# Kernel tuning notes

Measured on AMD Instinct MI355X. Metric: run time of the kernel, lower is better.

## Reference

```python
import jax, jax.numpy as jnp
import numpy as np

SIGMAS = (1.0, 2.0, 3.0, 4.0, 5.0)
ALPHAS = jnp.asarray([0.1, 0.2, 0.3, 0.4, 0.5], dtype=jnp.float32)
KSIZE = 7
PAD = KSIZE // 2  # 3, reflect padding


def _gaussian_kernels():
    # matches torch: x = arange(-ks//2+1, ks//2+1) = [-3..3]
    x = np.arange(-KSIZE // 2 + 1, KSIZE // 2 + 1, dtype=np.float32)
    ks = []
    for s in SIGMAS:
        g = np.exp(-x ** 2 / (2.0 * s ** 2))
        k = np.outer(g, g)
        k /= k.sum()
        ks.append(k)
    # depthwise conv kernels: (H, 1, 7, 7), OIHW with feature_group_count=H
    return jnp.asarray(np.stack(ks)[:, None, :, :])


def setup_inputs() -> dict:
    key = jax.random.key(0)
    ks = jax.random.split(key, 5)
    B, N, C = 8, 1024, 320
    return {
        "x": jax.random.normal(ks[0], (B, N, C), dtype=jnp.float32),
        "ln_g": jnp.ones((C,), dtype=jnp.float32),
        "ln_b": jnp.zeros((C,), dtype=jnp.float32),
        "qkv_w": jax.random.normal(ks[1], (3 * C, C), dtype=jnp.float32) * 0.02,
        "qkv_b": jax.random.normal(ks[2], (3 * C,), dtype=jnp.float32) * 0.02,
        "proj_w": jax.random.normal(ks[3], (C, C), dtype=jnp.float32) * 0.02,
        "proj_b": jax.random.normal(ks[4], (C,), dtype=jnp.float32) * 0.02,
    }


def reference(x, ln_g, ln_b, qkv_w, qkv_b, proj_w, proj_b):
    B, N, C = x.shape
    H = 5
    d = C // H
    kernels = _gaussian_kernels()  # (H,1,7,7), fixed buffers

    # LayerNorm
    mu = jnp.mean(x, axis=-1, keepdims=True)
    var = jnp.var(x, axis=-1, keepdims=True)
    xn = (x - mu) * jax.lax.rsqrt(var + 1e-5) * ln_g + ln_b

    # QKV projection -> (3, B, H, N, d)
    qkv = (xn @ qkv_w.T + qkv_b).reshape(B, N, 3, H, d).transpose(2, 0, 3, 1, 4)
    q, k, v = qkv[0], qkv[1], qkv[2]

    # attention scores (B, H, N, N)
    attn = jnp.einsum("bhnd,bhmd->bhnm", q, k) * (d ** -0.5)

    # per-head Gaussian blur as depthwise conv with reflect padding
    padded = jnp.pad(attn, ((0, 0), (0, 0), (PAD, PAD), (PAD, PAD)), mode="reflect")
    blurred = jax.lax.conv_general_dilated(
        padded, kernels, window_strides=(1, 1), padding="VALID",
        dimension_numbers=("NCHW", "OIHW", "NCHW"), feature_group_count=H)

    combined = jax.nn.softmax(attn + ALPHAS[None, :, None, None] * blurred, axis=-1)

    out = jnp.einsum("bhnm,bhmd->bhnd", combined, v)  # (B,H,N,d)
    out = out.transpose(0, 2, 1, 3).reshape(B, N, C)
    return out @ proj_w.T + proj_b
```

## Files before the change

### kernel.cpp

```cpp
#include <hip/hip_runtime.h>
#include <math.h>

#define B_ 8
#define N_ 1024
#define C_ 320
#define H_ 5
#define D_ 64
#define M_ (B_*N_)

typedef unsigned short ushort_t;
typedef _Float16 half_t;
typedef __attribute__((ext_vector_type(2))) _Float16 h2;
typedef __attribute__((ext_vector_type(8))) _Float16 f16x8;
typedef __attribute__((ext_vector_type(4))) float f32x4;

__device__ __forceinline__ ushort_t f2h(float f) {
  union { half_t h; ushort_t u; } c; c.h = (half_t)f; return c.u;
}
__device__ __forceinline__ unsigned pkrtz(float a, float b) {
  auto r = __builtin_amdgcn_cvt_pkrtz(a, b);
  union { decltype(r) v; unsigned u; } c; c.v = r; return c.u;
}

__global__ __launch_bounds__(256) void prep_kernel(
    const float* __restrict__ qkv_w, const float* __restrict__ proj_w,
    const float* __restrict__ x, const float* __restrict__ gamma,
    const float* __restrict__ beta,
    ushort_t* __restrict__ wqb, ushort_t* __restrict__ wpb,
    ushort_t* __restrict__ xnb) {
  int bid = blockIdx.x;
  int tid = threadIdx.x;
  if (bid < 200) {
    const float* src = bid < 150 ? qkv_w : proj_w;
    ushort_t* dst    = bid < 150 ? wqb   : wpb;
    int base = (bid < 150 ? bid : bid - 150) * 2048;
    int idx = base + tid*8;
    float4 x0 = *(const float4*)(src+idx);
    float4 x1 = *(const float4*)(src+idx+4);
    unsigned pk[4] = {pkrtz(x0.x,x0.y), pkrtz(x0.z,x0.w),
                      pkrtz(x1.x,x1.y), pkrtz(x1.z,x1.w)};
    *(uint4*)(dst+idx) = *(const uint4*)pk;
  } else {
    int row = (bid - 200)*4 + (tid >> 6);
    int lane = tid & 63;
    const float* xr = x + (long)row * C_;
    float vals[5];
    float s = 0.f, ss = 0.f;
#pragma unroll
    for (int j = 0; j < 5; ++j) {
      float vv = xr[lane + 64*j];
      vals[j] = vv; s += vv; ss += vv*vv;
    }
#pragma unroll
    for (int o = 32; o > 0; o >>= 1) {
      s  += __shfl_xor(s, o, 64);
      ss += __shfl_xor(ss, o, 64);
    }
    float mean = s * (1.0f/C_);
    float var  = ss * (1.0f/C_) - mean*mean;
    float rstd = rsqrtf(var + 1e-5f);
    ushort_t* outr = xnb + (long)row * C_;
#pragma unroll
    for (int j = 0; j < 5; ++j) {
      int c = lane + 64*j;
      outr[c] = f2h((vals[j]-mean)*rstd*gamma[c] + beta[c]);
    }
  }
}

__global__ __launch_bounds__(256) void qkvm_kernel(const ushort_t* __restrict__ xnb,
    const ushort_t* __restrict__ wqb, const float* __restrict__ bias,
    ushort_t* __restrict__ q, ushort_t* __restrict__ k, ushort_t* __restrict__ vt) {
  __shared__ __align__(16) ushort_t As[128][72];
  __shared__ __align__(16) ushort_t Bs[64][72];
  __shared__ __align__(16) ushort_t Vs[64][136];
  int j0 = blockIdx.x * 64;
  int m0 = blockIdx.y * 128;
  int tid = threadIdx.x;
  int lane = tid & 63, wv = tid >> 6;
  int l16 = lane & 15, qd = lane >> 4;
  f32x4 acc[2][4];
#pragma unroll
  for (int i=0;i<2;++i)
#pragma unroll
    for (int j=0;j<4;++j) acc[i][j] = (f32x4){0.f,0.f,0.f,0.f};
  for (int kk = 0; kk < C_; kk += 64) {
#pragma unroll
    for (int i = 0; i < 4; ++i) {
      int idx = tid + 256*i;
      int row = idx >> 3, c8 = (idx & 7) << 3;
      *(uint4*)&As[row][c8] = *(const uint4*)(xnb + (long)(m0+row)*C_ + kk + c8);
    }
    {
      int idx = tid;
      int row = idx >> 3, c8 = (idx & 7) << 3;
      *(uint4*)&Bs[row][c8] = *(const uint4*)(wqb + (long)(j0+row)*C_ + kk + c8);
      idx = tid + 256; row = idx >> 3; c8 = (idx & 7) << 3;
      *(uint4*)&Bs[row][c8] = *(const uint4*)(wqb + (long)(j0+row)*C_ + kk + c8);
    }
    __syncthreads();
#pragma unroll
    for (int kb = 0; kb < 2; ++kb) {
      int ko = kb*32 + qd*8;
      f16x8 a0 = *(const f16x8*)&As[wv*32 + l16][ko];
      f16x8 a1 = *(const f16x8*)&As[wv*32 + 16 + l16][ko];
#pragma unroll
      for (int ct = 0; ct < 4; ++ct) {
        f16x8 b = *(const f16x8*)&Bs[ct*16 + l16][ko];
        acc[0][ct] = __builtin_amdgcn_mfma_f32_16x16x32_f16(a0, b, acc[0][ct], 0,0,0);
        acc[1][ct] = __builtin_amdgcn_mfma_f32_16x16x32_f16(a1, b, acc[1][ct], 0,0,0);
      }
    }
    __syncthreads();
  }
  int three = j0 / 320;
  int rembase = j0 - three*320;
  if (three < 2) {
    ushort_t* dst = three == 0 ? q : k;
    float scale = three == 0 ? 0.125f : 1.0f;
#pragma unroll
    for (int rt = 0; rt < 2; ++rt)
#pragma unroll
      for (int ct = 0; ct < 4; ++ct) {
        int rem = rembase + ct*16 + l16;
        int h = rem >> 6, dd = rem & 63;
        float bi = bias[j0 + ct*16 + l16];
#pragma unroll
        for (int r = 0; r < 4; ++r) {
          int m = m0 + wv*32 + rt*16 + qd*4 + r;
          int b = m >> 10, n = m & (N_-1);
          dst[(((long)b*H_ + h)*N_ + n)*D_ + dd] = f2h((acc[rt][ct][r] + bi) * scale);
        }
      }
  } else {
    int h = rembase >> 6;
#pragma unroll
    for (int rt = 0; rt < 2; ++rt)
#pragma unroll
      for (int ct = 0; ct < 4; ++ct) {
        float bi = bias[j0 + ct*16 + l16];
#pragma unroll
        for (int r = 0; r < 4; ++r) {
          int col = wv*32 + rt*16 + qd*4 + r;
          Vs[ct*16 + l16][col] = f2h(acc[rt][ct][r] + bi);
        }
      }
    __syncthreads();
    int b = m0 >> 10, n0b = m0 & (N_-1);
#pragma unroll
    for (int i = 0; i < 4; ++i) {
      int idx = tid + 256*i;
      int row = idx >> 4, c8 = (idx & 15) << 3;
      *(uint4*)(vt + (((long)b*H_ + h)*D_ + row)*N_ + n0b + c8) = *(const uint4*)&Vs[row][c8];
    }
  }
}

__global__ __launch_bounds__(512) void qb_kernel(
    const ushort_t* __restrict__ q, const ushort_t* __restrict__ kk,
    ushort_t* __restrict__ qb, ushort_t* __restrict__ kb) {
  int bh = blockIdx.y;
  int h = bh % H_;
  int r = blockIdx.x*64 + (threadIdx.x >> 3);
  int d8 = (threadIdx.x & 7) << 3;
  float sigma = (float)(h + 1);
  float ei = -1.f / (2.f * sigma * sigma);
  float ga = expf(9.f*ei), gb = expf(4.f*ei), gc = expf(1.f*ei);
  float isum = 1.f / (2.f*(ga + gb + gc) + 1.f);
  float alpha = 0.1f * sigma;
  const float w[7] = {ga*isum, gb*isum, gc*isum, isum, gc*isum, gb*isum, ga*isum};
  const ushort_t* qb_base = q  + (long)bh*N_*D_ + d8;
  const ushort_t* kb_base = kk + (long)bh*N_*D_ + d8;
  float aq[8] = {0,0,0,0,0,0,0,0};
  float ak[8] = {0,0,0,0,0,0,0,0};
#pragma unroll
  for (int t = 0; t < 7; ++t) {
    int p = r + t - 3;
    int rr = p < 0 ? -p : (p > N_-1 ? 2*(N_-1)-p : p);
    union { uint4 v; h2 hh[4]; } uq, uk;
    uq.v = *(const uint4*)(qb_base + (long)rr*D_);
    uk.v = *(const uint4*)(kb_base + (long)rr*D_);
    float wt = w[t];
#pragma unroll
    for (int j = 0; j < 4; ++j) {
      aq[2*j]   += wt * (float)uq.hh[j].x;
      aq[2*j+1] += wt * (float)uq.hh[j].y;
      ak[2*j]   += wt * (float)uk.hh[j].x;
      ak[2*j+1] += wt * (float)uk.hh[j].y;
    }
  }
  ushort_t pq[8], pk[8];
#pragma unroll
  for (int j = 0; j < 8; ++j) {
    pq[j] = f2h(aq[j]);
    pk[j] = f2h(ak[j] * alpha);
  }
  long ooff = ((long)bh*N_ + r)*D_ + d8;
  *(uint4*)(qb + ooff) = *(const uint4*)pq;
  *(uint4*)(kb + ooff) = *(const uint4*)pk;
}

__global__ __launch_bounds__(256, 2) void bsp_kernel(
    const ushort_t* __restrict__ q,  const ushort_t* __restrict__ qbb,
    const ushort_t* __restrict__ kk, const ushort_t* __restrict__ kb,
    const ushort_t* __restrict__ vt, ushort_t* __restrict__ aob) {
  __shared__ __align__(16) ushort_t Ks[2][64][72];
  __shared__ __align__(16) ushort_t Bs[2][64][72];
  __shared__ __align__(16) ushort_t Vs[2][64][72];
  __shared__ __align__(16) ushort_t Pb[4][16][72];

  int lin = blockIdx.x;
  int lin2 = (lin & 7)*80 + (lin >> 3);
  int bh = lin2 >> 4;
  int qblk = lin2 & 15;
  int h = bh % H_;
  int bb = bh / H_;
  int tid = threadIdx.x;
  int wv = tid >> 6, lane = tid & 63;
  int l16 = lane & 15, qd = lane >> 4;
  int qbase = qblk*64 + wv*16;

  int srow = tid >> 3, sc8 = (tid & 7) << 3;
  const ushort_t* kgp = kk + (long)bh*N_*D_ + (long)srow*D_ + sc8;
  const ushort_t* bgp = kb + (long)bh*N_*D_ + (long)srow*D_ + sc8;
  const ushort_t* vgp = vt + (long)bh*D_*N_ + (long)srow*N_ + sc8;

  long qoff = ((long)bh*N_ + qbase + l16)*D_ + qd*8;
  f16x8 bq0 = *(const f16x8*)(q   + qoff);
  f16x8 bq1 = *(const f16x8*)(q   + qoff + 32);
  f16x8 bq2 = *(const f16x8*)(qbb + qoff);
  f16x8 bq3 = *(const f16x8*)(qbb + qoff + 32);

  ushort_t (*Pw)[72] = Pb[wv];
  float rsum = 0.f;
  f32x4 oa[4];
#pragma unroll
  for (int dt = 0; dt < 4; ++dt) oa[dt] = (f32x4){0.f,0.f,0.f,0.f};

  {
    uint4 k0 = *(const uint4*)(kgp);
    uint4 k1 = *(const uint4*)(kgp + 32*D_);
    uint4 b0 = *(const uint4*)(bgp);
    uint4 b1 = *(const uint4*)(bgp + 32*D_);
    uint4 v0 = *(const uint4*)(vgp);
    uint4 v1 = *(const uint4*)(vgp + 32*N_);
    *(uint4*)&Ks[0][srow][sc8]    = k0;
    *(uint4*)&Ks[0][srow+32][sc8] = k1;
    *(uint4*)&Bs[0][srow][sc8]    = b0;
    *(uint4*)&Bs[0][srow+32][sc8] = b1;
    *(uint4*)&Vs[0][srow][sc8]    = v0;
    *(uint4*)&Vs[0][srow+32][sc8] = v1;
  }
  __syncthreads();

  for (int ch = 0; ch < 16; ++ch) {
    const int cur = ch & 1, nxt = cur ^ 1;
    uint4 gk0, gk1, gb0, gb1, gv0, gv1;
    if (ch < 15) {
      int c1 = (ch + 1) * 64;
      gk0 = *(const uint4*)(kgp + (long)c1*D_);
      gk1 = *(const uint4*)(kgp + (long)(c1+32)*D_);
      gb0 = *(const uint4*)(bgp + (long)c1*D_);
      gb1 = *(const uint4*)(bgp + (long)(c1+32)*D_);
      gv0 = *(const uint4*)(vgp + c1);
      gv1 = *(const uint4*)(vgp + 32*N_ + c1);
    }
#pragma unroll
    for (int kt = 0; kt < 4; ++kt) {
      int r = kt*16 + l16;
      f16x8 a0 = *(const f16x8*)&Ks[cur][r][qd*8];
      f16x8 a1 = *(const f16x8*)&Ks[cur][r][qd*8 + 32];
      f16x8 a2 = *(const f16x8*)&Bs[cur][r][qd*8];
      f16x8 a3 = *(const f16x8*)&Bs[cur][r][qd*8 + 32];
      f32x4 s = (f32x4){0.f,0.f,0.f,0.f};
      s = __builtin_amdgcn_mfma_f32_16x16x32_f16(a0, bq0, s, 0,0,0);
      s = __builtin_amdgcn_mfma_f32_16x16x32_f16(a1, bq1, s, 0,0,0);
      s = __builtin_amdgcn_mfma_f32_16x16x32_f16(a2, bq2, s, 0,0,0);
      s = __builtin_amdgcn_mfma_f32_16x16x32_f16(a3, bq3, s, 0,0,0);
      float e0 = __expf(s[0]), e1 = __expf(s[1]);
      float e2 = __expf(s[2]), e3 = __expf(s[3]);
      rsum += (e0 + e1) + (e2 + e3);
      *(uint2*)&Pw[l16][kt*16 + qd*4] = make_uint2(pkrtz(e0,e1), pkrtz(e2,e3));
    }
#pragma unroll
    for (int ks = 0; ks < 2; ++ks) {
      f16x8 af = *(const f16x8*)&Pw[l16][ks*32 + qd*8];
#pragma unroll
      for (int dt = 0; dt < 4; ++dt) {
        f16x8 bf = *(const f16x8*)&Vs[cur][dt*16 + l16][ks*32 + qd*8];
        oa[dt] = __builtin_amdgcn_mfma_f32_16x16x32_f16(af, bf, oa[dt], 0,0,0);
      }
    }
    if (ch < 15) {
      *(uint4*)&Ks[nxt][srow][sc8]    = gk0;
      *(uint4*)&Ks[nxt][srow+32][sc8] = gk1;
      *(uint4*)&Bs[nxt][srow][sc8]    = gb0;
      *(uint4*)&Bs[nxt][srow+32][sc8] = gb1;
      *(uint4*)&Vs[nxt][srow][sc8]    = gv0;
      *(uint4*)&Vs[nxt][srow+32][sc8] = gv1;
    }
    __syncthreads();
  }

  rsum += __shfl_xor(rsum, 16, 64);
  rsum += __shfl_xor(rsum, 32, 64);
  float rinv = 1.f / rsum;
  float rv[4];
#pragma unroll
  for (int r = 0; r < 4; ++r) rv[r] = __shfl(rinv, qd*4 + r, 64);
#pragma unroll
  for (int dt = 0; dt < 4; ++dt)
#pragma unroll
    for (int r = 0; r < 4; ++r)
      aob[((long)(bb*N_ + qbase + qd*4 + r))*C_ + h*64 + dt*16 + l16] =
          f2h(oa[dt][r] * rv[r]);
}

__global__ __launch_bounds__(256) void projm_kernel(const ushort_t* __restrict__ aob,
    const ushort_t* __restrict__ wpb, const float* __restrict__ bias,
    float* __restrict__ out) {
  __shared__ __align__(16) ushort_t As[128][72];
  __shared__ __align__(16) ushort_t Bs[64][72];
  int j0 = blockIdx.x * 64;
  int m0 = blockIdx.y * 128;
  int tid = threadIdx.x;
  int lane = tid & 63, wv = tid >> 6;
  int l16 = lane & 15, qd = lane >> 4;
  f32x4 acc[2][4];
#pragma unroll
  for (int i=0;i<2;++i)
#pragma unroll
    for (int j=0;j<4;++j) acc[i][j] = (f32x4){0.f,0.f,0.f,0.f};
  for (int kk = 0; kk < C_; kk += 64) {
#pragma unroll
    for (int i = 0; i < 4; ++i) {
      int idx = tid + 256*i;
      int row = idx >> 3, c8 = (idx & 7) << 3;
      *(uint4*)&As[row][c8] = *(const uint4*)(aob + (long)(m0+row)*C_ + kk + c8);
    }
    {
      int idx = tid;
      int row = idx >> 3, c8 = (idx & 7) << 3;
      *(uint4*)&Bs[row][c8] = *(const uint4*)(wpb + (long)(j0+row)*C_ + kk + c8);
      idx = tid + 256; row = idx >> 3; c8 = (idx & 7) << 3;
      *(uint4*)&Bs[row][c8] = *(const uint4*)(wpb + (long)(j0+row)*C_ + kk + c8);
    }
    __syncthreads();
#pragma unroll
    for (int kb = 0; kb < 2; ++kb) {
      int ko = kb*32 + qd*8;
      f16x8 a0 = *(const f16x8*)&As[wv*32 + l16][ko];
      f16x8 a1 = *(const f16x8*)&As[wv*32 + 16 + l16][ko];
#pragma unroll
      for (int ct = 0; ct < 4; ++ct) {
        f16x8 b = *(const f16x8*)&Bs[ct*16 + l16][ko];
        acc[0][ct] = __builtin_amdgcn_mfma_f32_16x16x32_f16(a0, b, acc[0][ct], 0,0,0);
        acc[1][ct] = __builtin_amdgcn_mfma_f32_16x16x32_f16(a1, b, acc[1][ct], 0,0,0);
      }
    }
    __syncthreads();
  }
#pragma unroll
  for (int rt = 0; rt < 2; ++rt)
#pragma unroll
    for (int ct = 0; ct < 4; ++ct) {
      float bi = bias[j0 + ct*16 + l16];
#pragma unroll
      for (int r = 0; r < 4; ++r) {
        int m = m0 + wv*32 + rt*16 + qd*4 + r;
        out[(long)m*C_ + j0 + ct*16 + l16] = acc[rt][ct][r] + bi;
      }
    }
}

extern "C" void kernel_launch(void* const* d_in, const int* in_sizes, int n_in,
                              void* d_out, int out_size, void* d_ws, size_t ws_size,
                              hipStream_t stream) {
  const float* x      = (const float*)d_in[0];
  const float* ln_g   = (const float*)d_in[1];
  const float* ln_b   = (const float*)d_in[2];
  const float* qkv_w  = (const float*)d_in[3];
  const float* qkv_b  = (const float*)d_in[4];
  const float* proj_w = (const float*)d_in[5];
  const float* proj_b = (const float*)d_in[6];
  float* out = (float*)d_out;

  char* ws = (char*)d_ws;
  const long sz_bhnd = (long)B_*H_*N_*D_;
  ushort_t* xnb  = (ushort_t*)ws;                   ws += (long)M_*C_*2;
  ushort_t* aob  = (ushort_t*)ws;                   ws += (long)M_*C_*2;
  ushort_t* q    = (ushort_t*)ws;                   ws += sz_bhnd*2;
  ushort_t* k    = (ushort_t*)ws;                   ws += sz_bhnd*2;
  ushort_t* vt   = (ushort_t*)ws;                   ws += sz_bhnd*2;
  ushort_t* qb   = (ushort_t*)ws;                   ws += sz_bhnd*2;
  ushort_t* kb   = (ushort_t*)ws;                   ws += sz_bhnd*2;
  ushort_t* wqb  = (ushort_t*)ws;                   ws += (long)3*C_*C_*2;
  ushort_t* wpb  = (ushort_t*)ws;                   ws += (long)C_*C_*2;

  prep_kernel<<<2248, 256, 0, stream>>>(qkv_w, proj_w, x, ln_g, ln_b, wqb, wpb, xnb);
  qkvm_kernel<<<dim3(15, 64), 256, 0, stream>>>(xnb, wqb, qkv_b, q, k, vt);
  qb_kernel<<<dim3(16, B_*H_), 512, 0, stream>>>(q, k, qb, kb);
  bsp_kernel<<<640, 256, 0, stream>>>(q, qb, k, kb, vt, aob);
  projm_kernel<<<dim3(5, 64), 256, 0, stream>>>(aob, wpb, proj_b, out);
}
```

Measured before the change: 139.2 us.

## Register-prefetch GEMM tiles and single-buffer attention LDS for higher occupancy

Result: slower. 188.7 us (+35.6%).

```diff
diff --git a/kernel.cpp b/kernel.cpp
--- a/kernel.cpp
+++ b/kernel.cpp
@@ -84,19 +84,46 @@
   for (int i=0;i<2;++i)
 #pragma unroll
     for (int j=0;j<4;++j) acc[i][j] = (f32x4){0.f,0.f,0.f,0.f};
-  for (int kk = 0; kk < C_; kk += 64) {
+
+  uint4 rA[4], rB[2];
+#pragma unroll
+  for (int i = 0; i < 4; ++i) {
+    int idx = tid + 256*i;
+    int row = idx >> 3, c8 = (idx & 7) << 3;
+    rA[i] = *(const uint4*)(xnb + (long)(m0+row)*C_ + c8);
+  }
+  {
+    int idx = tid, row = idx >> 3, c8 = (idx & 7) << 3;
+    rB[0] = *(const uint4*)(wqb + (long)(j0+row)*C_ + c8);
+    idx = tid + 256; row = idx >> 3; c8 = (idx & 7) << 3;
+    rB[1] = *(const uint4*)(wqb + (long)(j0+row)*C_ + c8);
+  }
+  for (int kt5 = 0; kt5 < 5; ++kt5) {
+    __syncthreads();
 #pragma unroll
     for (int i = 0; i < 4; ++i) {
       int idx = tid + 256*i;
       int row = idx >> 3, c8 = (idx & 7) << 3;
-      *(uint4*)&As[row][c8] = *(const uint4*)(xnb + (long)(m0+row)*C_ + kk + c8);
+      *(uint4*)&As[row][c8] = rA[i];
     }
     {
-      int idx = tid;
-      int row = idx >> 3, c8 = (idx & 7) << 3;
-      *(uint4*)&Bs[row][c8] = *(const uint4*)(wqb + (long)(j0+row)*C_ + kk + c8);
+      int idx = tid, row = idx >> 3, c8 = (idx & 7) << 3;
+      *(uint4*)&Bs[row][c8] = rB[0];
       idx = tid + 256; row = idx >> 3; c8 = (idx & 7) << 3;
-      *(uint4*)&Bs[row][c8] = *(const uint4*)(wqb + (long)(j0+row)*C_ + kk + c8);
+      *(uint4*)&Bs[row][c8] = rB[1];
+    }
+    if (kt5 < 4) {
+      int kn = kt5*64 + 64;
+#pragma unroll
+      for (int i = 0; i < 4; ++i) {
+        int idx = tid + 256*i;
+        int row = idx >> 3, c8 = (idx & 7) << 3;
+        rA[i] = *(const uint4*)(xnb + (long)(m0+row)*C_ + kn + c8);
+      }
+      int idx = tid, row = idx >> 3, c8 = (idx & 7) << 3;
+      rB[0] = *(const uint4*)(wqb + (long)(j0+row)*C_ + kn + c8);
+      idx = tid + 256; row = idx >> 3; c8 = (idx & 7) << 3;
+      rB[1] = *(const uint4*)(wqb + (long)(j0+row)*C_ + kn + c8);
     }
     __syncthreads();
 #pragma unroll
@@ -111,7 +138,6 @@
         acc[1][ct] = __builtin_amdgcn_mfma_f32_16x16x32_f16(a1, b, acc[1][ct], 0,0,0);
       }
     }
-    __syncthreads();
   }
   int three = j0 / 320;
   int rembase = j0 - three*320;
@@ -134,6 +160,7 @@
       }
   } else {
     int h = rembase >> 6;
+    __syncthreads();
 #pragma unroll
     for (int rt = 0; rt < 2; ++rt)
 #pragma unroll
@@ -200,13 +227,13 @@
   *(uint4*)(kb + ooff) = *(const uint4*)pk;
 }
 
-__global__ __launch_bounds__(256, 2) void bsp_kernel(
+__global__ __launch_bounds__(256, 4) void bsp_kernel(
     const ushort_t* __restrict__ q,  const ushort_t* __restrict__ qbb,
     const ushort_t* __restrict__ kk, const ushort_t* __restrict__ kb,
     const ushort_t* __restrict__ vt, ushort_t* __restrict__ aob) {
-  __shared__ __align__(16) ushort_t Ks[2][64][72];
-  __shared__ __align__(16) ushort_t Bs[2][64][72];
-  __shared__ __align__(16) ushort_t Vs[2][64][72];
+  __shared__ __align__(16) ushort_t Ks[64][72];
+  __shared__ __align__(16) ushort_t Bs[64][72];
+  __shared__ __align__(16) ushort_t Vs[64][72];
   __shared__ __align__(16) ushort_t Pb[4][16][72];
 
   int lin = blockIdx.x;
@@ -237,24 +264,15 @@
 #pragma unroll
   for (int dt = 0; dt < 4; ++dt) oa[dt] = (f32x4){0.f,0.f,0.f,0.f};
 
-  {
-    uint4 k0 = *(const uint4*)(kgp);
-    uint4 k1 = *(const uint4*)(kgp + 32*D_);
-    uint4 b0 = *(const uint4*)(bgp);
-    uint4 b1 = *(const uint4*)(bgp + 32*D_);
-    uint4 v0 = *(const uint4*)(vgp);
-    uint4 v1 = *(const uint4*)(vgp + 32*N_);
-    *(uint4*)&Ks[0][srow][sc8]    = k0;
-    *(uint4*)&Ks[0][srow+32][sc8] = k1;
-    *(uint4*)&Bs[0][srow][sc8]    = b0;
-    *(uint4*)&Bs[0][srow+32][sc8] = b1;
-    *(uint4*)&Vs[0][srow][sc8]    = v0;
-    *(uint4*)&Vs[0][srow+32][sc8] = v1;
-  }
+  *(uint4*)&Ks[srow][sc8]    = *(const uint4*)(kgp);
+  *(uint4*)&Ks[srow+32][sc8] = *(const uint4*)(kgp + 32*D_);
+  *(uint4*)&Bs[srow][sc8]    = *(const uint4*)(bgp);
+  *(uint4*)&Bs[srow+32][sc8] = *(const uint4*)(bgp + 32*D_);
+  *(uint4*)&Vs[srow][sc8]    = *(const uint4*)(vgp);
+  *(uint4*)&Vs[srow+32][sc8] = *(const uint4*)(vgp + 32*N_);
   __syncthreads();
 
   for (int ch = 0; ch < 16; ++ch) {
-    const int cur = ch & 1, nxt = cur ^ 1;
     uint4 gk0, gk1, gb0, gb1, gv0, gv1;
     if (ch < 15) {
       int c1 = (ch + 1) * 64;
@@ -268,10 +286,10 @@
 #pragma unroll
     for (int kt = 0; kt < 4; ++kt) {
       int r = kt*16 + l16;
-      f16x8 a0 = *(const f16x8*)&Ks[cur][r][qd*8];
-      f16x8 a1 = *(const f16x8*)&Ks[cur][r][qd*8 + 32];
-      f16x8 a2 = *(const f16x8*)&Bs[cur][r][qd*8];
-      f16x8 a3 = *(const f16x8*)&Bs[cur][r][qd*8 + 32];
+      f16x8 a0 = *(const f16x8*)&Ks[r][qd*8];
+      f16x8 a1 = *(const f16x8*)&Ks[r][qd*8 + 32];
+      f16x8 a2 = *(const f16x8*)&Bs[r][qd*8];
+      f16x8 a3 = *(const f16x8*)&Bs[r][qd*8 + 32];
       f32x4 s = (f32x4){0.f,0.f,0.f,0.f};
       s = __builtin_amdgcn_mfma_f32_16x16x32_f16(a0, bq0, s, 0,0,0);
       s = __builtin_amdgcn_mfma_f32_16x16x32_f16(a1, bq1, s, 0,0,0);
@@ -287,19 +305,20 @@
       f16x8 af = *(const f16x8*)&Pw[l16][ks*32 + qd*8];
 #pragma unroll
       for (int dt = 0; dt < 4; ++dt) {
-        f16x8 bf = *(const f16x8*)&Vs[cur][dt*16 + l16][ks*32 + qd*8];
+        f16x8 bf = *(const f16x8*)&Vs[dt*16 + l16][ks*32 + qd*8];
         oa[dt] = __builtin_amdgcn_mfma_f32_16x16x32_f16(af, bf, oa[dt], 0,0,0);
       }
     }
     if (ch < 15) {
-      *(uint4*)&Ks[nxt][srow][sc8]    = gk0;
-      *(uint4*)&Ks[nxt][srow+32][sc8] = gk1;
-      *(uint4*)&Bs[nxt][srow][sc8]    = gb0;
-      *(uint4*)&Bs[nxt][srow+32][sc8] = gb1;
-      *(uint4*)&Vs[nxt][srow][sc8]    = gv0;
-      *(uint4*)&Vs[nxt][srow+32][sc8] = gv1;
-    }
-    __syncthreads();
+      __syncthreads();
+      *(uint4*)&Ks[srow][sc8]    = gk0;
+      *(uint4*)&Ks[srow+32][sc8] = gk1;
+      *(uint4*)&Bs[srow][sc8]    = gb0;
+      *(uint4*)&Bs[srow+32][sc8] = gb1;
+      *(uint4*)&Vs[srow][sc8]    = gv0;
+      *(uint4*)&Vs[srow+32][sc8] = gv1;
+      __syncthreads();
+    }
   }
 
   rsum += __shfl_xor(rsum, 16, 64);
@@ -331,19 +350,46 @@
   for (int i=0;i<2;++i)
 #pragma unroll
     for (int j=0;j<4;++j) acc[i][j] = (f32x4){0.f,0.f,0.f,0.f};
-  for (int kk = 0; kk < C_; kk += 64) {
+
+  uint4 rA[4], rB[2];
+#pragma unroll
+  for (int i = 0; i < 4; ++i) {
+    int idx = tid + 256*i;
+    int row = idx >> 3, c8 = (idx & 7) << 3;
+    rA[i] = *(const uint4*)(aob + (long)(m0+row)*C_ + c8);
+  }
+  {
+    int idx = tid, row = idx >> 3, c8 = (idx & 7) << 3;
+    rB[0] = *(const uint4*)(wpb + (long)(j0+row)*C_ + c8);
+    idx = tid + 256; row = idx >> 3; c8 = (idx & 7) << 3;
+    rB[1] = *(const uint4*)(wpb + (long)(j0+row)*C_ + c8);
+  }
+  for (int kt5 = 0; kt5 < 5; ++kt5) {
+    __syncthreads();
 #pragma unroll
     for (int i = 0; i < 4; ++i) {
       int idx = tid + 256*i;
       int row = idx >> 3, c8 = (idx & 7) << 3;
-      *(uint4*)&As[row][c8] = *(const uint4*)(aob + (long)(m0+row)*C_ + kk + c8);
+      *(uint4*)&As[row][c8] = rA[i];
     }
     {
-      int idx = tid;
-      int row = idx >> 3, c8 = (idx & 7) << 3;
-      *(uint4*)&Bs[row][c8] = *(const uint4*)(wpb + (long)(j0+row)*C_ + kk + c8);
+      int idx = tid, row = idx >> 3, c8 = (idx & 7) << 3;
+      *(uint4*)&Bs[row][c8] = rB[0];
       idx = tid + 256; row = idx >> 3; c8 = (idx & 7) << 3;
-      *(uint4*)&Bs[row][c8] = *(const uint4*)(wpb + (long)(j0+row)*C_ + kk + c8);
+      *(uint4*)&Bs[row][c8] = rB[1];
+    }
+    if (kt5 < 4) {
+      int kn = kt5*64 + 64;
+#pragma unroll
+      for (int i = 0; i < 4; ++i) {
+        int idx = tid + 256*i;
+        int row = idx >> 3, c8 = (idx & 7) << 3;
+        rA[i] = *(const uint4*)(aob + (long)(m0+row)*C_ + kn + c8);
+      }
+      int idx = tid, row = idx >> 3, c8 = (idx & 7) << 3;
+      rB[0] = *(const uint4*)(wpb + (long)(j0+row)*C_ + kn + c8);
+      idx = tid + 256; row = idx >> 3; c8 = (idx & 7) << 3;
+      rB[1] = *(const uint4*)(wpb + (long)(j0+row)*C_ + kn + c8);
     }
     __syncthreads();
 #pragma unroll
@@ -358,7 +404,6 @@
         acc[1][ct] = __builtin_amdgcn_mfma_f32_16x16x32_f16(a1, b, acc[1][ct], 0,0,0);
       }
     }
-    __syncthreads();
   }
 #pragma unroll
   for (int rt = 0; rt < 2; ++rt)
```

## Load QKV and projection GEMM operands directly from global memory, dropping LDS staging

Applied to the files above, without the earlier changes.

New measurement: 163.6 us. +17.5%, slower.

```diff
diff --git a/kernel.cpp b/kernel.cpp
--- a/kernel.cpp
+++ b/kernel.cpp
@@ -71,8 +71,6 @@
 __global__ __launch_bounds__(256) void qkvm_kernel(const ushort_t* __restrict__ xnb,
     const ushort_t* __restrict__ wqb, const float* __restrict__ bias,
     ushort_t* __restrict__ q, ushort_t* __restrict__ k, ushort_t* __restrict__ vt) {
-  __shared__ __align__(16) ushort_t As[128][72];
-  __shared__ __align__(16) ushort_t Bs[64][72];
   __shared__ __align__(16) ushort_t Vs[64][136];
   int j0 = blockIdx.x * 64;
   int m0 = blockIdx.y * 128;
@@ -84,34 +82,25 @@
   for (int i=0;i<2;++i)
 #pragma unroll
     for (int j=0;j<4;++j) acc[i][j] = (f32x4){0.f,0.f,0.f,0.f};
-  for (int kk = 0; kk < C_; kk += 64) {
-#pragma unroll
-    for (int i = 0; i < 4; ++i) {
-      int idx = tid + 256*i;
-      int row = idx >> 3, c8 = (idx & 7) << 3;
-      *(uint4*)&As[row][c8] = *(const uint4*)(xnb + (long)(m0+row)*C_ + kk + c8);
-    }
-    {
-      int idx = tid;
-      int row = idx >> 3, c8 = (idx & 7) << 3;
-      *(uint4*)&Bs[row][c8] = *(const uint4*)(wqb + (long)(j0+row)*C_ + kk + c8);
-      idx = tid + 256; row = idx >> 3; c8 = (idx & 7) << 3;
-      *(uint4*)&Bs[row][c8] = *(const uint4*)(wqb + (long)(j0+row)*C_ + kk + c8);
-    }
-    __syncthreads();
+
+  const ushort_t* a0p = xnb + (long)(m0 + wv*32 + l16)*C_ + qd*8;
+  const ushort_t* a1p = a0p + 16*C_;
+  const ushort_t* b0p = wqb + (long)(j0 + l16)*C_ + qd*8;
+
+#pragma unroll
+  for (int kk5 = 0; kk5 < 5; ++kk5) {
 #pragma unroll
     for (int kb = 0; kb < 2; ++kb) {
-      int ko = kb*32 + qd*8;
-      f16x8 a0 = *(const f16x8*)&As[wv*32 + l16][ko];
-      f16x8 a1 = *(const f16x8*)&As[wv*32 + 16 + l16][ko];
+      int ko = kk5*64 + kb*32;
+      f16x8 a0 = *(const f16x8*)(a0p + ko);
+      f16x8 a1 = *(const f16x8*)(a1p + ko);
 #pragma unroll
       for (int ct = 0; ct < 4; ++ct) {
-        f16x8 b = *(const f16x8*)&Bs[ct*16 + l16][ko];
+        f16x8 b = *(const f16x8*)(b0p + (long)ct*16*C_ + ko);
         acc[0][ct] = __builtin_amdgcn_mfma_f32_16x16x32_f16(a0, b, acc[0][ct], 0,0,0);
         acc[1][ct] = __builtin_amdgcn_mfma_f32_16x16x32_f16(a1, b, acc[1][ct], 0,0,0);
       }
     }
-    __syncthreads();
   }
   int three = j0 / 320;
   int rembase = j0 - three*320;
@@ -319,8 +308,6 @@
 __global__ __launch_bounds__(256) void projm_kernel(const ushort_t* __restrict__ aob,
     const ushort_t* __restrict__ wpb, const float* __restrict__ bias,
     float* __restrict__ out) {
-  __shared__ __align__(16) ushort_t As[128][72];
-  __shared__ __align__(16) ushort_t Bs[64][72];
   int j0 = blockIdx.x * 64;
   int m0 = blockIdx.y * 128;
   int tid = threadIdx.x;
@@ -331,34 +318,25 @@
   for (int i=0;i<2;++i)
 #pragma unroll
     for (int j=0;j<4;++j) acc[i][j] = (f32x4){0.f,0.f,0.f,0.f};
-  for (int kk = 0; kk < C_; kk += 64) {
-#pragma unroll
-    for (int i = 0; i < 4; ++i) {
-      int idx = tid + 256*i;
-      int row = idx >> 3, c8 = (idx & 7) << 3;
-      *(uint4*)&As[row][c8] = *(const uint4*)(aob + (long)(m0+row)*C_ + kk + c8);
-    }
-    {
-      int idx = tid;
-      int row = idx >> 3, c8 = (idx & 7) << 3;
-      *(uint4*)&Bs[row][c8] = *(const uint4*)(wpb + (long)(j0+row)*C_ + kk + c8);
-      idx = tid + 256; row = idx >> 3; c8 = (idx & 7) << 3;
-      *(uint4*)&Bs[row][c8] = *(const uint4*)(wpb + (long)(j0+row)*C_ + kk + c8);
-    }
-    __syncthreads();
+
+  const ushort_t* a0p = aob + (long)(m0 + wv*32 + l16)*C_ + qd*8;
+  const ushort_t* a1p = a0p + 16*C_;
+  const ushort_t* b0p = wpb + (long)(j0 + l16)*C_ + qd*8;
+
+#pragma unroll
+  for (int kk5 = 0; kk5 < 5; ++kk5) {
 #pragma unroll
     for (int kb = 0; kb < 2; ++kb) {
-      int ko = kb*32 + qd*8;
-      f16x8 a0 = *(const f16x8*)&As[wv*32 + l16][ko];
-      f16x8 a1 = *(const f16x8*)&As[wv*32 + 16 + l16][ko];
+      int ko = kk5*64 + kb*32;
+      f16x8 a0 = *(const f16x8*)(a0p + ko);
+      f16x8 a1 = *(const f16x8*)(a1p + ko);
 #pragma unroll
       for (int ct = 0; ct < 4; ++ct) {
-        f16x8 b = *(const f16x8*)&Bs[ct*16 + l16][ko];
+        f16x8 b = *(const f16x8*)(b0p + (long)ct*16*C_ + ko);
         acc[0][ct] = __builtin_amdgcn_mfma_f32_16x16x32_f16(a0, b, acc[0][ct], 0,0,0);
         acc[1][ct] = __builtin_amdgcn_mfma_f32_16x16x32_f16(a1, b, acc[1][ct], 0,0,0);
       }
     }
-    __syncthreads();
   }
 #pragma unroll
   for (int rt = 0; rt < 2; ++rt)
```
